# Performance work log

Measured on AMD Instinct MI355X. Metric: run time of the kernel, lower is better.

## Reference

```python
import jax, jax.numpy as jnp
import numpy as np

B, T, W = 256, 1024, 512   # batch, input length, input width (channels)
U, P = 512, 16             # rnn units, psc kernel length


def setup_inputs() -> dict:
    key = jax.random.key(0)
    ks = jax.random.split(key, 6)
    # spike-like input raster (original uses Bernoulli(0.1); uniform floats keep identical math)
    x = jax.random.uniform(ks[0], (B, T, W), dtype=jnp.float32)
    # shared per-channel Conv1D(filters=1, kernel_size=P): kernel (P,) + scalar bias
    psc_w = jax.random.normal(ks[1], (P,), dtype=jnp.float32) * (1.0 / np.sqrt(P))
    psc_b = jax.random.normal(ks[2], (1,), dtype=jnp.float32) * 0.01
    # SimpleRNNCell(units, activation=None) weights
    kernel = jax.random.normal(ks[3], (W, U), dtype=jnp.float32) * (1.0 / np.sqrt(W))
    rec_kernel = jax.random.normal(ks[4], (U, U), dtype=jnp.float32) * (1.0 / np.sqrt(U))
    bias = jax.random.normal(ks[5], (U,), dtype=jnp.float32) * 0.01
    return {"x": x, "psc_w": psc_w, "psc_b": psc_b, "kernel": kernel,
            "rec_kernel": rec_kernel, "bias": bias}


def reference(x, psc_w, psc_b, kernel, rec_kernel, bias):
    # --- psc: one shared Conv1D(1, P, valid) applied independently to every channel ---
    # Original loops channels and concatenates; equivalent to a depthwise conv with
    # a single shared (P,) kernel along time. Express as a sum over P shifted slices.
    Bn, Tn, Wn = x.shape
    Pn = psc_w.shape[0]
    Tp = Tn - Pn + 1
    syn = psc_b[0] + sum(psc_w[k] * x[:, k:k + Tp, :] for k in range(Pn))  # (B, Tp, W)

    # --- sequential spiking RNN: SimpleRNNCell(activation=None) + sigmoid spike/reset ---
    def step(state, s_t):
        # linear cell: out = s_t @ K + state @ R + b
        out = s_t @ kernel + state @ rec_kernel + bias        # (B, U)
        n = jax.nn.sigmoid(3.0 * out)                          # spike output
        new_state = out * jax.nn.sigmoid(2.0 * (0.5 - n))      # soft reset gating
        return new_state, n

    syn_t = jnp.swapaxes(syn, 0, 1)                            # (Tp, B, W)
    state0 = jnp.zeros((Bn, bias.shape[0]), dtype=x.dtype)
    _, ns = jax.lax.scan(step, state0, syn_t)                  # ns: (Tp, B, U)
    return jnp.swapaxes(ns, 0, 1)                              # (B, Tp, U)
```

## Files before the change

kernel.cpp:

```cpp
#include <hip/hip_runtime.h>
#include <hip/hip_fp16.h>
#include <cstdint>
#include <cstddef>

typedef _Float16 f16;
typedef __attribute__((ext_vector_type(8))) _Float16 f16x8;
typedef __attribute__((ext_vector_type(4))) _Float16 f16x4;
typedef __attribute__((ext_vector_type(2))) _Float16 f16x2;
typedef __attribute__((ext_vector_type(4))) float f32x4;

#define B_SZ 256
#define T_IN 1024
#define W_CH 512
#define U_N  512
#define P_K  16
#define TP   1009
#define MROWS (B_SZ * TP)

__global__ __launch_bounds__(256) void k_convert(
    const float* __restrict__ kern, const float* __restrict__ rec,
    f16* __restrict__ Kt, f16* __restrict__ Rt) {
  int idx = blockIdx.x * 256 + threadIdx.x;
  int which = idx >> 18;
  int e = idx & 262143;
  int n = e >> 9;
  int k = e & 511;
  if (which == 0) {
    Kt[(size_t)n * 512 + k] = (f16)kern[(size_t)k * 512 + n];
  } else {
    int kp = (k & 448) | ((k & 15) << 2) | ((k >> 4) & 3);
    Rt[(size_t)n * 512 + kp] = (f16)rec[(size_t)k * 512 + n];
  }
}

__global__ __launch_bounds__(256) void k_conv(
    const float* __restrict__ x, const float* __restrict__ psc_w,
    const float* __restrict__ psc_b, f16* __restrict__ syn) {
  int g  = blockIdx.x * 256 + threadIdx.x;
  int wq = g & 127;
  int tt = (g >> 7) & 15;
  int b  = g >> 11;
  int t0 = tt * 64;
  const float4* xr = (const float4*)x + (size_t)b * T_IN * 128 + wq;
  float wgt[16];
#pragma unroll
  for (int k = 0; k < 16; ++k) wgt[k] = psc_w[k];
  float b0 = psc_b[0];
  float4 win[16];
#pragma unroll
  for (int i = 0; i < 15; ++i) win[i] = xr[(size_t)(t0 + i) * 128];
  f16* sp = syn + ((size_t)b * TP + t0) * 512 + wq * 4;
  int steps = TP - t0; if (steps > 64) steps = 64;
  for (int j0 = 0; j0 < 64; j0 += 16) {
#pragma unroll
    for (int jj = 0; jj < 16; ++jj) {
      int j = j0 + jj;
      if (j < steps) {
        win[(j + 15) & 15] = xr[(size_t)(t0 + j + 15) * 128];
        float ax = b0, ay = b0, az = b0, aw = b0;
#pragma unroll
        for (int k = 0; k < 16; ++k) {
          float4 v = win[(j + k) & 15];
          float wk = wgt[k];
          ax += wk * v.x; ay += wk * v.y; az += wk * v.z; aw += wk * v.w;
        }
        f16x4 o; o.x = (f16)ax; o.y = (f16)ay; o.z = (f16)az; o.w = (f16)aw;
        *(f16x4*)(sp + (size_t)j * 512) = o;
      }
    }
  }
}

__global__ __launch_bounds__(256) void k_gemm(
    const f16* __restrict__ syn, const f16* __restrict__ Kt,
    const float* __restrict__ bias, float* __restrict__ out) {
  int bid = blockIdx.x;
  size_t m0 = (size_t)(bid >> 2) * 128;
  int n0 = (bid & 3) * 128;
  int tid = threadIdx.x;
  int wave = tid >> 6, lane = tid & 63;
  int q = lane >> 4, l15 = lane & 15;
  __shared__ f16 lA[128 * 32];
  __shared__ f16 lB[128 * 32];
  f32x4 acc[8][2] = {};
  int s0 = tid, s1 = tid + 256;
  int rA0 = s0 >> 2, cA0 = (s0 & 3) * 8;
  int rA1 = s1 >> 2, cA1 = (s1 & 3) * 8;
  for (int k0 = 0; k0 < 512; k0 += 32) {
    f16x8 a0 = *(const f16x8*)(syn + (m0 + rA0) * 512 + k0 + cA0);
    f16x8 a1 = *(const f16x8*)(syn + (m0 + rA1) * 512 + k0 + cA1);
    f16x8 b0 = *(const f16x8*)(Kt + (size_t)(n0 + rA0) * 512 + k0 + cA0);
    f16x8 b1 = *(const f16x8*)(Kt + (size_t)(n0 + rA1) * 512 + k0 + cA1);
    __syncthreads();
    *(f16x8*)(lA + s0 * 8) = a0;  *(f16x8*)(lA + s1 * 8) = a1;
    *(f16x8*)(lB + s0 * 8) = b0;  *(f16x8*)(lB + s1 * 8) = b1;
    __syncthreads();
    f16x8 bf[2];
#pragma unroll
    for (int j = 0; j < 2; ++j)
      bf[j] = *(const f16x8*)(lB + (wave * 32 + j * 16 + l15) * 32 + q * 8);
#pragma unroll
    for (int i = 0; i < 8; ++i) {
      f16x8 af = *(const f16x8*)(lA + (i * 16 + l15) * 32 + q * 8);
      acc[i][0] = __builtin_amdgcn_mfma_f32_16x16x32_f16(af, bf[0], acc[i][0], 0, 0, 0);
      acc[i][1] = __builtin_amdgcn_mfma_f32_16x16x32_f16(af, bf[1], acc[i][1], 0, 0, 0);
    }
  }
#pragma unroll
  for (int j = 0; j < 2; ++j) {
    int col = n0 + wave * 32 + j * 16 + l15;
    float bv = bias[col];
#pragma unroll
    for (int i = 0; i < 8; ++i) {
      size_t row = m0 + i * 16 + q * 4;
#pragma unroll
      for (int r = 0; r < 4; ++r)
        out[(row + r) * 512 + col] = acc[i][j][r] + bv;
    }
  }
}

__global__ __launch_bounds__(1024, 4) void k_rnn(
    const f16* __restrict__ Rt, float* __restrict__ io) {
  int b = blockIdx.x;
  int tid = threadIdx.x, wave = tid >> 6, lane = tid & 63;
  int q = lane >> 4, l15 = lane & 15;
  __shared__ f16 R4[4 * 512 * 32];
  __shared__ __align__(64) f16 SRZ[1600];

  {
    int row = tid & 511;
    int h = tid >> 9;
    const f16x8* src = (const f16x8*)(Rt + (size_t)row * 512 + 11 * 32);
#pragma unroll
    for (int gg = 0; gg < 2; ++gg) {
      int g = h * 2 + gg;
      char* dst = (char*)R4 + g * 32768 + row * 64;
#pragma unroll
      for (int c = 0; c < 4; ++c)
        *(f16x8*)(dst + ((c * 16) ^ ((row & 3) << 4))) = src[g * 4 + c];
    }
    for (int i = tid; i < 1600; i += 1024) SRZ[i] = (f16)0.f;
  }

  int row0 = wave * 32 + l15;
  const f16* rbase = Rt + (size_t)row0 * 512 + q * 8;
  f16x8 rs[11][2];
#pragma unroll
  for (int kk = 0; kk < 11; ++kk)
#pragma unroll
    for (int nt = 0; nt < 2; ++nt)
      rs[kk][nt] = *(const f16x8*)(rbase + (size_t)nt * 8192 + kk * 32);

  const char* r4base = (const char*)R4 + row0 * 64
                       + ((q * 16) ^ ((l15 & 3) << 4));

  bool l0 = (l15 == 0);
  const f16* zb = SRZ + 1056 + q * 8;
  const f16* pc = l0 ? (SRZ + q * 8)       : zb;
  const f16* pn = l0 ? (SRZ + 512 + q * 8) : zb;
  int wpos = (wave >> 1) * 64 + l15 * 4 + 2 * (wave & 1);
  f16* wc = SRZ + 512 + wpos;
  f16* wn = SRZ + wpos;

  bool active = (q == 0);
  unsigned ioff = (unsigned)b * (TP * 512u) + (unsigned)row0;
  float xp0 = io[ioff], xp1 = io[ioff + 16u];

  __syncthreads();

  for (int t = 0; t < TP; ++t) {
    f16x8 sw0 = *(const f16x8*)(rbase + 15 * 32);
    f16x8 sw1 = *(const f16x8*)(rbase + 8192 + 15 * 32);
    f32x4 a0 = {}, a1 = {};
#pragma unroll
    for (int kk = 0; kk < 11; ++kk) {
      f16x8 af = *(const f16x8*)(pc + kk * 32);
      a0 = __builtin_amdgcn_mfma_f32_16x16x32_f16(af, rs[kk][0], a0, 0, 0, 0);
      a1 = __builtin_amdgcn_mfma_f32_16x16x32_f16(af, rs[kk][1], a1, 0, 0, 0);
    }
#pragma unroll
    for (int g = 0; g < 4; ++g) {
      f16x8 bf0 = *(const f16x8*)(r4base + g * 32768);
      f16x8 bf1 = *(const f16x8*)(r4base + g * 32768 + 1024);
      f16x8 af  = *(const f16x8*)(pc + (11 + g) * 32);
      a0 = __builtin_amdgcn_mfma_f32_16x16x32_f16(af, bf0, a0, 0, 0, 0);
      a1 = __builtin_amdgcn_mfma_f32_16x16x32_f16(af, bf1, a1, 0, 0, 0);
    }
    {
      f16x8 af = *(const f16x8*)(pc + 15 * 32);
      a0 = __builtin_amdgcn_mfma_f32_16x16x32_f16(af, sw0, a0, 0, 0, 0);
      a1 = __builtin_amdgcn_mfma_f32_16x16x32_f16(af, sw1, a1, 0, 0, 0);
    }
    {
      float o0 = a0[0] + xp0;
      float o1 = a1[0] + xp1;
      float n0 = __builtin_amdgcn_rcpf(1.f + __builtin_amdgcn_exp2f(-4.3280850f * o0));
      float n1 = __builtin_amdgcn_rcpf(1.f + __builtin_amdgcn_exp2f(-4.3280850f * o1));
      float g0 = __builtin_amdgcn_rcpf(1.f + __builtin_amdgcn_exp2f((2.f * n0 - 1.f) * 1.4426950f));
      float g1 = __builtin_amdgcn_rcpf(1.f + __builtin_amdgcn_exp2f((2.f * n1 - 1.f) * 1.4426950f));
      if (active) {
        io[ioff]       = n0;
        io[ioff + 16u] = n1;
        f16x2 sv; sv.x = (f16)(o0 * g0); sv.y = (f16)(o1 * g1);
        *(f16x2*)wc = sv;
      }
    }
    ioff += 512u;
    if (t < TP - 1) {
      xp0 = io[ioff]; xp1 = io[ioff + 16u];
    }
    asm volatile("s_waitcnt lgkmcnt(0)\n\ts_barrier" ::: "memory");
    const f16* tp = pc; pc = pn; pn = tp;
    f16* tw = wc; wc = wn; wn = tw;
  }
}

extern "C" void kernel_launch(void* const* d_in, const int* in_sizes, int n_in,
                              void* d_out, int out_size, void* d_ws, size_t ws_size,
                              hipStream_t stream) {
  (void)in_sizes; (void)n_in; (void)out_size; (void)ws_size;
  const float* x     = (const float*)d_in[0];
  const float* psc_w = (const float*)d_in[1];
  const float* psc_b = (const float*)d_in[2];
  const float* kern  = (const float*)d_in[3];
  const float* rec   = (const float*)d_in[4];
  const float* bias  = (const float*)d_in[5];
  float* out = (float*)d_out;
  char* ws = (char*)d_ws;
  f16* syn = (f16*)ws;
  f16* Kt  = (f16*)(ws + 264503296ull);
  f16* Rt  = (f16*)(ws + 265027584ull);

  k_convert<<<2048, 256, 0, stream>>>(kern, rec, Kt, Rt);
  k_conv   <<<2048, 256, 0, stream>>>(x, psc_w, psc_b, syn);
  k_gemm   <<<2018 * 4, 256, 0, stream>>>(syn, Kt, bias, out);
  k_rnn    <<<256, 1024, 0, stream>>>(Rt, out);
}
```

Baseline: 2.607 ms.

## Rebalance RNN recurrent weights across registers, global streaming and LDS

Reduces register-resident recurrent-weight slices from 11 to 8 K-chunks. Four chunks (12-15) are now streamed from global/L2 each step, double-buffered and prefetched across the barrier. The LDS-resident chunks move to K 8-11. Activation fragments are loaded only by lane-0 rows into registers (others stay zero), replacing the padded zero-buffer trick and interleaving loads with MFMAs. The intent is to lower register pressure and hide weight and LDS latency in the serial time loop, at the cost of more global weight traffic per step.

Result: slower. 3.913 ms (+50.1%).

```diff
diff --git a/kernel.cpp b/kernel.cpp
--- a/kernel.cpp
+++ b/kernel.cpp
@@ -126,12 +126,12 @@
   int tid = threadIdx.x, wave = tid >> 6, lane = tid & 63;
   int q = lane >> 4, l15 = lane & 15;
   __shared__ f16 R4[4 * 512 * 32];
-  __shared__ __align__(64) f16 SRZ[1600];
+  __shared__ f16 SR[2 * 512];
 
   {
     int row = tid & 511;
     int h = tid >> 9;
-    const f16x8* src = (const f16x8*)(Rt + (size_t)row * 512 + 11 * 32);
+    const f16x8* src = (const f16x8*)(Rt + (size_t)row * 512 + 8 * 32);
 #pragma unroll
     for (int gg = 0; gg < 2; ++gg) {
       int g = h * 2 + gg;
@@ -140,14 +140,14 @@
       for (int c = 0; c < 4; ++c)
         *(f16x8*)(dst + ((c * 16) ^ ((row & 3) << 4))) = src[g * 4 + c];
     }
-    for (int i = tid; i < 1600; i += 1024) SRZ[i] = (f16)0.f;
+    if (tid < 512) { SR[tid] = (f16)0.f; SR[512 + tid] = (f16)0.f; }
   }
 
   int row0 = wave * 32 + l15;
   const f16* rbase = Rt + (size_t)row0 * 512 + q * 8;
-  f16x8 rs[11][2];
-#pragma unroll
-  for (int kk = 0; kk < 11; ++kk)
+  f16x8 rs[8][2];
+#pragma unroll
+  for (int kk = 0; kk < 8; ++kk)
 #pragma unroll
     for (int nt = 0; nt < 2; ++nt)
       rs[kk][nt] = *(const f16x8*)(rbase + (size_t)nt * 8192 + kk * 32);
@@ -156,41 +156,82 @@
                        + ((q * 16) ^ ((l15 & 3) << 4));
 
   bool l0 = (l15 == 0);
-  const f16* zb = SRZ + 1056 + q * 8;
-  const f16* pc = l0 ? (SRZ + q * 8)       : zb;
-  const f16* pn = l0 ? (SRZ + 512 + q * 8) : zb;
+  bool active = (q == 0);
+
+  f16x8 afr[4];
+#pragma unroll
+  for (int i = 0; i < 4; ++i) afr[i] = (f16x8){};
+
+  const f16* pc = SR + q * 8;
+  const f16* pn = SR + 512 + q * 8;
   int wpos = (wave >> 1) * 64 + l15 * 4 + 2 * (wave & 1);
-  f16* wc = SRZ + 512 + wpos;
-  f16* wn = SRZ + wpos;
-
-  bool active = (q == 0);
+  f16* wc = SR + 512 + wpos;
+  f16* wn = SR + wpos;
+
   unsigned ioff = (unsigned)b * (TP * 512u) + (unsigned)row0;
   float xp0 = io[ioff], xp1 = io[ioff + 16u];
 
+  f16x8 swA[2], swB[2];
+  swA[0] = *(const f16x8*)(rbase + 12 * 32);
+  swA[1] = *(const f16x8*)(rbase + 8192 + 12 * 32);
+  swB[0] = *(const f16x8*)(rbase + 13 * 32);
+  swB[1] = *(const f16x8*)(rbase + 8192 + 13 * 32);
+
   __syncthreads();
 
   for (int t = 0; t < TP; ++t) {
-    f16x8 sw0 = *(const f16x8*)(rbase + 15 * 32);
-    f16x8 sw1 = *(const f16x8*)(rbase + 8192 + 15 * 32);
     f32x4 a0 = {}, a1 = {};
-#pragma unroll
-    for (int kk = 0; kk < 11; ++kk) {
-      f16x8 af = *(const f16x8*)(pc + kk * 32);
-      a0 = __builtin_amdgcn_mfma_f32_16x16x32_f16(af, rs[kk][0], a0, 0, 0, 0);
-      a1 = __builtin_amdgcn_mfma_f32_16x16x32_f16(af, rs[kk][1], a1, 0, 0, 0);
+    if (l0) {
+#pragma unroll
+      for (int i = 0; i < 4; ++i) afr[i] = *(const f16x8*)(pc + i * 32);
+    }
+#pragma unroll
+    for (int kk = 0; kk < 4; ++kk) {
+      a0 = __builtin_amdgcn_mfma_f32_16x16x32_f16(afr[kk], rs[kk][0], a0, 0, 0, 0);
+      a1 = __builtin_amdgcn_mfma_f32_16x16x32_f16(afr[kk], rs[kk][1], a1, 0, 0, 0);
+    }
+    if (l0) {
+      afr[0] = *(const f16x8*)(pc + 12 * 32);
+      afr[1] = *(const f16x8*)(pc + 13 * 32);
+      afr[2] = *(const f16x8*)(pc + 4 * 32);
+      afr[3] = *(const f16x8*)(pc + 5 * 32);
+    }
+    a0 = __builtin_amdgcn_mfma_f32_16x16x32_f16(afr[0], swA[0], a0, 0, 0, 0);
+    a1 = __builtin_amdgcn_mfma_f32_16x16x32_f16(afr[0], swA[1], a1, 0, 0, 0);
+    a0 = __builtin_amdgcn_mfma_f32_16x16x32_f16(afr[1], swB[0], a0, 0, 0, 0);
+    a1 = __builtin_amdgcn_mfma_f32_16x16x32_f16(afr[1], swB[1], a1, 0, 0, 0);
+    swA[0] = *(const f16x8*)(rbase + 14 * 32);
+    swA[1] = *(const f16x8*)(rbase + 8192 + 14 * 32);
+    swB[0] = *(const f16x8*)(rbase + 15 * 32);
+    swB[1] = *(const f16x8*)(rbase + 8192 + 15 * 32);
+    a0 = __builtin_amdgcn_mfma_f32_16x16x32_f16(afr[2], rs[4][0], a0, 0, 0, 0);
+    a1 = __builtin_amdgcn_mfma_f32_16x16x32_f16(afr[2], rs[4][1], a1, 0, 0, 0);
+    a0 = __builtin_amdgcn_mfma_f32_16x16x32_f16(afr[3], rs[5][0], a0, 0, 0, 0);
+    a1 = __builtin_amdgcn_mfma_f32_16x16x32_f16(afr[3], rs[5][1], a1, 0, 0, 0);
+    if (l0) {
+      afr[0] = *(const f16x8*)(pc + 6 * 32);
+      afr[1] = *(const f16x8*)(pc + 7 * 32);
+      afr[2] = *(const f16x8*)(pc + 14 * 32);
+      afr[3] = *(const f16x8*)(pc + 15 * 32);
+    }
+    a0 = __builtin_amdgcn_mfma_f32_16x16x32_f16(afr[0], rs[6][0], a0, 0, 0, 0);
+    a1 = __builtin_amdgcn_mfma_f32_16x16x32_f16(afr[0], rs[6][1], a1, 0, 0, 0);
+    a0 = __builtin_amdgcn_mfma_f32_16x16x32_f16(afr[1], rs[7][0], a0, 0, 0, 0);
+    a1 = __builtin_amdgcn_mfma_f32_16x16x32_f16(afr[1], rs[7][1], a1, 0, 0, 0);
+    a0 = __builtin_amdgcn_mfma_f32_16x16x32_f16(afr[2], swA[0], a0, 0, 0, 0);
+    a1 = __builtin_amdgcn_mfma_f32_16x16x32_f16(afr[2], swA[1], a1, 0, 0, 0);
+    a0 = __builtin_amdgcn_mfma_f32_16x16x32_f16(afr[3], swB[0], a0, 0, 0, 0);
+    a1 = __builtin_amdgcn_mfma_f32_16x16x32_f16(afr[3], swB[1], a1, 0, 0, 0);
+    if (l0) {
+#pragma unroll
+      for (int i = 0; i < 4; ++i) afr[i] = *(const f16x8*)(pc + (8 + i) * 32);
     }
 #pragma unroll
     for (int g = 0; g < 4; ++g) {
       f16x8 bf0 = *(const f16x8*)(r4base + g * 32768);
       f16x8 bf1 = *(const f16x8*)(r4base + g * 32768 + 1024);
-      f16x8 af  = *(const f16x8*)(pc + (11 + g) * 32);
-      a0 = __builtin_amdgcn_mfma_f32_16x16x32_f16(af, bf0, a0, 0, 0, 0);
-      a1 = __builtin_amdgcn_mfma_f32_16x16x32_f16(af, bf1, a1, 0, 0, 0);
-    }
-    {
-      f16x8 af = *(const f16x8*)(pc + 15 * 32);
-      a0 = __builtin_amdgcn_mfma_f32_16x16x32_f16(af, sw0, a0, 0, 0, 0);
-      a1 = __builtin_amdgcn_mfma_f32_16x16x32_f16(af, sw1, a1, 0, 0, 0);
+      a0 = __builtin_amdgcn_mfma_f32_16x16x32_f16(afr[g], bf0, a0, 0, 0, 0);
+      a1 = __builtin_amdgcn_mfma_f32_16x16x32_f16(afr[g], bf1, a1, 0, 0, 0);
     }
     {
       float o0 = a0[0] + xp0;
@@ -209,6 +250,10 @@
     ioff += 512u;
     if (t < TP - 1) {
       xp0 = io[ioff]; xp1 = io[ioff + 16u];
+      swA[0] = *(const f16x8*)(rbase + 12 * 32);
+      swA[1] = *(const f16x8*)(rbase + 8192 + 12 * 32);
+      swB[0] = *(const f16x8*)(rbase + 13 * 32);
+      swB[1] = *(const f16x8*)(rbase + 8192 + 13 * 32);
     }
     asm volatile("s_waitcnt lgkmcnt(0)\n\ts_barrier" ::: "memory");
     const f16* tp = pc; pc = pn; pn = tp;
```
